# Kernel tuning notes

Measured on AMD Instinct MI355X. Metric: run time of the kernel, lower is better.

## Reference

```python
import jax, jax.numpy as jnp
import numpy as np

N = 6144
F_IN, H1, H2, EMB = 512, 256, 128, 64
ALPHA = 0.2  # LeakyReLU negative slope
NEG_INF = -9e15


def setup_inputs() -> dict:
    key = jax.random.key(0)
    ks = jax.random.split(key, 12)
    x = jax.random.normal(ks[0], (N, F_IN), dtype=jnp.float32)
    adj = (jax.random.uniform(ks[1], (N, N)) < 0.01).astype(jnp.float32)
    adj = jnp.maximum(adj, jnp.eye(N, dtype=jnp.float32))
    M = jax.random.uniform(ks[2], (N, N), dtype=jnp.float32)

    def glorot(k, shape):
        lim = float(np.sqrt(6.0 / (shape[0] + shape[1])))
        return jax.random.uniform(k, shape, jnp.float32, -lim, lim)

    params = {
        "W1": glorot(ks[3], (F_IN, H1)), "a_s1": glorot(ks[4], (H1, 1)), "a_n1": glorot(ks[5], (H1, 1)),
        "W2": glorot(ks[6], (H1, H2)),  "a_s2": glorot(ks[7], (H2, 1)), "a_n2": glorot(ks[8], (H2, 1)),
        "W3": glorot(ks[9], (H2, EMB)), "a_s3": glorot(ks[10], (EMB, 1)), "a_n3": glorot(ks[11], (EMB, 1)),
    }
    return {"x": x, "adj": adj, "M": M, **params}


def _gat_layer(x, adj, M, W, a_s, a_n):
    h = x @ W                                   # [N, d_out]
    e = (h @ a_s) + (h @ a_n).T                 # [N, N] pairwise logits
    e = jax.nn.leaky_relu(e * M, ALPHA)
    e = jnp.where(adj > 0, e, NEG_INF)
    att = jax.nn.softmax(e, axis=1)             # masked row softmax
    return jax.nn.elu(att @ h)


def reference(x, adj, M, W1, a_s1, a_n1, W2, a_s2, a_n2, W3, a_s3, a_n3):
    h = _gat_layer(x, adj, M, W1, a_s1, a_n1)
    h = _gat_layer(h, adj, M, W2, a_s2, a_n2)
    h = _gat_layer(h, adj, M, W3, a_s3, a_n3)
    z = h / jnp.maximum(jnp.linalg.norm(h, axis=1, keepdims=True), 1e-12)
    A_pred = jax.nn.sigmoid(z @ z.T)
    return (A_pred, z)
```

## Files before the change

### kernel.cpp

```cpp
#include <hip/hip_runtime.h>
#include <hip/hip_bf16.h>
#include <math.h>

#define NROW 6144
#define LRELU_ALPHA 0.2f
#define MAXD 128

typedef __attribute__((ext_vector_type(8))) __bf16 bf16x8;
typedef __attribute__((ext_vector_type(16))) float f32x16;

__global__ __launch_bounds__(256) void prep_scan(
    const float* __restrict__ adj, uint32_t* __restrict__ bm,
    const float* __restrict__ W1, const float* __restrict__ W2, const float* __restrict__ W3,
    __bf16* __restrict__ w1h, __bf16* __restrict__ w1l,
    __bf16* __restrict__ w2h, __bf16* __restrict__ w2l,
    __bf16* __restrict__ w3h, __bf16* __restrict__ w3l,
    const float* __restrict__ as1, const float* __restrict__ an1,
    const float* __restrict__ as2, const float* __restrict__ an2,
    const float* __restrict__ as3, const float* __restrict__ an3,
    float* __restrict__ wsa1, float* __restrict__ wna1,
    float* __restrict__ wsa2, float* __restrict__ wna2,
    float* __restrict__ wsa3, float* __restrict__ wna3) {
  int b = blockIdx.x;
  if (b < NROW) {
    const int id = b * 256 + threadIdx.x;
    const int row = id >> 8, sub = id & 255;
    const float4* ap = (const float4*)(adj + (size_t)row * NROW) + (sub >> 6) * 384 + (sub & 63);
    uint32_t mk = 0;
#pragma unroll
    for (int it = 0; it < 6; ++it) {
      float4 a = ap[it * 64];
      uint32_t q = (uint32_t)(a.x > 0.f) | ((uint32_t)(a.y > 0.f) << 1) |
                   ((uint32_t)(a.z > 0.f) << 2) | ((uint32_t)(a.w > 0.f) << 3);
      mk |= q << (it * 4);
    }
    bm[id] = mk;
    return;
  }
  b -= NROW;
  if (b < 672) {
    int idx = b * 256 + threadIdx.x;
    const float* W; __bf16 *wh, *wl; int K, D;
    if (idx < 131072) { W = W1; wh = w1h; wl = w1l; K = 512; D = 256; }
    else if (idx < 163840) { idx -= 131072; W = W2; wh = w2h; wl = w2l; K = 256; D = 128; }
    else { idx -= 163840; if (idx >= 8192) return; W = W3; wh = w3h; wl = w3l; K = 128; D = 64; }
    int k = idx / D, d = idx - k * D;
    float v = W[idx];
    __bf16 h = (__bf16)v;
    wh[(size_t)d * K + k] = h;
    wl[(size_t)d * K + k] = (__bf16)(v - (float)h);
    return;
  }
  int t = (b - 672) * 256 + threadIdx.x;
  if (t < 512) {
    float s = 0.f, n = 0.f;
    for (int d = 0; d < 256; ++d) { float w = W1[t * 256 + d]; s = fmaf(w, as1[d], s); n = fmaf(w, an1[d], n); }
    wsa1[t] = s; wna1[t] = n;
  } else if (t < 768) {
    int k = t - 512;
    float s = 0.f, n = 0.f;
    for (int d = 0; d < 128; ++d) { float w = W2[k * 128 + d]; s = fmaf(w, as2[d], s); n = fmaf(w, an2[d], n); }
    wsa2[k] = s; wna2[k] = n;
  } else if (t < 896) {
    int k = t - 768;
    float s = 0.f, n = 0.f;
    for (int d = 0; d < 64; ++d) { float w = W3[k * 64 + d]; s = fmaf(w, as3[d], s); n = fmaf(w, an3[d], n); }
    wsa3[k] = s; wna3[k] = n;
  }
}

__global__ __launch_bounds__(256) void csr_from_bitmap(const uint32_t* __restrict__ bm,
                                                       const float* __restrict__ Mm,
                                                       int* __restrict__ cnt,
                                                       int* __restrict__ cidx,
                                                       float* __restrict__ cmval) {
  const int row = blockIdx.x;
  const int tid = threadIdx.x, wv = tid >> 6, lane = tid & 63;
  __shared__ int wtot[4];
  __shared__ int jsh[MAXD];
  const uint32_t mask = bm[row * 256 + tid];
  const int pc = __popc(mask);
  int pre = pc;
#pragma unroll
  for (int off = 1; off < 64; off <<= 1) {
    int t = __shfl_up(pre, off);
    if (lane >= off) pre += t;
  }
  if (lane == 63) wtot[wv] = pre;
  __syncthreads();
  int base = pre - pc;
  for (int w = 0; w < wv; ++w) base += wtot[w];
  const int total = min(wtot[0] + wtot[1] + wtot[2] + wtot[3], MAXD);
  uint32_t m = mask;
  int p = base;
  const int cb0 = wv * 1536 + lane * 4;
  while (m) {
    int bit = __ffs(m) - 1;
    m &= m - 1;
    if (p < MAXD) jsh[p] = cb0 + ((bit >> 2) << 8) + (bit & 3);
    ++p;
  }
  __syncthreads();
  const float* mrow = Mm + (size_t)row * NROW;
  for (int k = tid; k < total; k += 256) {
    int j = jsh[k];
    cidx[(size_t)row * MAXD + k] = j;
    cmval[(size_t)row * MAXD + k] = mrow[j];
  }
  if (tid == 0) cnt[row] = total;
}

__global__ __launch_bounds__(256) void gemm_lds(
    const float* __restrict__ A,
    const __bf16* __restrict__ Bth, const __bf16* __restrict__ Btl,
    const float* __restrict__ wsa, const float* __restrict__ wna,
    float* __restrict__ sv, float* __restrict__ nv,
    float* __restrict__ C, __bf16* __restrict__ Cb, int K, int D) {
  __shared__ __bf16 Ah[64][72], Al[64][72], Bh[64][72], Bl[64][72];
  const int tid = threadIdx.x;
  const int wv = tid >> 6, lane = tid & 63;
  const int l31 = lane & 31, lh = lane >> 5;
  const int wr = wv >> 1, wc = wv & 1;
  const int rb = blockIdx.x * 64, jb = blockIdx.y * 64;
  const bool do_sn = (blockIdx.y == 0) && (wc == 0);
  f32x16 acc;
#pragma unroll
  for (int r = 0; r < 16; ++r) acc[r] = 0.f;
  float ss = 0.f, nn = 0.f;
  for (int kt = 0; kt < K; kt += 64) {
#pragma unroll
    for (int c2 = 0; c2 < 4; ++c2) {
      int flat = c2 * 256 + tid;
      int row = flat >> 4, cq = (flat & 15) * 4;
      float4 a = *(const float4*)(A + (size_t)(rb + row) * K + kt + cq);
      __bf16 h0 = (__bf16)a.x, h1 = (__bf16)a.y, h2 = (__bf16)a.z, h3 = (__bf16)a.w;
      Ah[row][cq] = h0; Ah[row][cq + 1] = h1; Ah[row][cq + 2] = h2; Ah[row][cq + 3] = h3;
      Al[row][cq] = (__bf16)(a.x - (float)h0);
      Al[row][cq + 1] = (__bf16)(a.y - (float)h1);
      Al[row][cq + 2] = (__bf16)(a.z - (float)h2);
      Al[row][cq + 3] = (__bf16)(a.w - (float)h3);
    }
#pragma unroll
    for (int c2 = 0; c2 < 2; ++c2) {
      int flat = c2 * 256 + tid;
      int row = flat >> 3, cq = (flat & 7) * 8;
      *(bf16x8*)&Bh[row][cq] = *(const bf16x8*)(Bth + (size_t)(jb + row) * K + kt + cq);
      *(bf16x8*)&Bl[row][cq] = *(const bf16x8*)(Btl + (size_t)(jb + row) * K + kt + cq);
    }
    __syncthreads();
#pragma unroll
    for (int kk = 0; kk < 4; ++kk) {
      bf16x8 af  = *(const bf16x8*)&Ah[wr * 32 + l31][kk * 16 + lh * 8];
      bf16x8 alf = *(const bf16x8*)&Al[wr * 32 + l31][kk * 16 + lh * 8];
      bf16x8 bhf = *(const bf16x8*)&Bh[wc * 32 + l31][kk * 16 + lh * 8];
      bf16x8 blf = *(const bf16x8*)&Bl[wc * 32 + l31][kk * 16 + lh * 8];
      if (do_sn) {
        const float* wsp = wsa + kt + kk * 16 + lh * 8;
        const float* wnp = wna + kt + kk * 16 + lh * 8;
#pragma unroll
        for (int t = 0; t < 8; ++t) {
          float av = (float)af[t] + (float)alf[t];
          ss = fmaf(av, wsp[t], ss);
          nn = fmaf(av, wnp[t], nn);
        }
      }
      acc = __builtin_amdgcn_mfma_f32_32x32x16_bf16(af, bhf, acc, 0, 0, 0);
      acc = __builtin_amdgcn_mfma_f32_32x32x16_bf16(af, blf, acc, 0, 0, 0);
      acc = __builtin_amdgcn_mfma_f32_32x32x16_bf16(alf, bhf, acc, 0, 0, 0);
    }
    __syncthreads();
  }
  if (do_sn) {
    ss += __shfl_xor(ss, 32);
    nn += __shfl_xor(nn, 32);
    if (lh == 0) { sv[rb + wr * 32 + l31] = ss; nv[rb + wr * 32 + l31] = nn; }
  }
#pragma unroll
  for (int r = 0; r < 16; ++r) {
    int rowi = (r & 3) + 8 * (r >> 2) + 4 * lh + wr * 32;
    int col = jb + wc * 32 + l31;
    if (C)  C[(size_t)(rb + rowi) * D + col] = acc[r];
    if (Cb) Cb[(size_t)(rb + rowi) * D + col] = (__bf16)acc[r];
  }
}

template <int D, int WPR, bool BF16G, bool NORM>
__global__ __launch_bounds__(256) void attn_csr(const float* __restrict__ h,
                                                const __bf16* __restrict__ hb,
                                                const int* __restrict__ cnt,
                                                const int* __restrict__ cidx,
                                                const float* __restrict__ cmval,
                                                const float* __restrict__ sv,
                                                const float* __restrict__ nv,
                                                float* __restrict__ out,
                                                __bf16* __restrict__ zb) {
  constexpr int RPB = 4 / WPR;
  constexpr int CW = D / WPR;
  constexpr int NQ = BF16G ? 2 : CW / 64;
  __shared__ float ws[4][MAXD];
  __shared__ int js[4][MAXD];
  const int wv = threadIdx.x >> 6, lane = threadIdx.x & 63;
  const int row = blockIdx.x * RPB + wv / WPR;
  const int half = wv % WPR;
  const int c = cnt[row];
  const float si = sv[row];
  const size_t cb = (size_t)row * MAXD;

  float e0 = -1e30f, e1 = -1e30f;
  int j0 = 0, j1 = 0;
  if (lane < c) {
    j0 = cidx[cb + lane];
    float v = (si + nv[j0]) * cmval[cb + lane];
    e0 = v > 0.f ? v : LRELU_ALPHA * v;
  }
  if (lane + 64 < c) {
    j1 = cidx[cb + lane + 64];
    float v = (si + nv[j1]) * cmval[cb + lane + 64];
    e1 = v > 0.f ? v : LRELU_ALPHA * v;
  }
  float mx = fmaxf(e0, e1);
#pragma unroll
  for (int off = 32; off; off >>= 1) mx = fmaxf(mx, __shfl_xor(mx, off));
  float w0 = lane < c ? __expf(e0 - mx) : 0.f;
  float w1 = lane + 64 < c ? __expf(e1 - mx) : 0.f;
  float s = w0 + w1;
#pragma unroll
  for (int off = 32; off; off >>= 1) s += __shfl_xor(s, off);
  const float inv = 1.f / s;
  ws[wv][lane] = w0 * inv;
  ws[wv][lane + 64] = w1 * inv;
  js[wv][lane] = j0;
  js[wv][lane + 64] = j1;
  const int cbase = half * CW;
  float acc[NQ];
#pragma unroll
  for (int q = 0; q < NQ; ++q) acc[q] = 0.f;
  if (BF16G) {
#pragma unroll 8
    for (int k = 0; k < c; ++k) {
      const float wk = ws[wv][k];
      const uint32_t* hr = (const uint32_t*)(hb + (size_t)js[wv][k] * D + cbase);
      uint32_t v = hr[lane];
      acc[0] = fmaf(wk, __uint_as_float(v << 16), acc[0]);
      acc[1] = fmaf(wk, __uint_as_float(v & 0xffff0000u), acc[1]);
    }
    float2 o;
    o.x = acc[0] > 0.f ? acc[0] : expm1f(acc[0]);
    o.y = acc[1] > 0.f ? acc[1] : expm1f(acc[1]);
    *(float2*)(out + (size_t)row * D + cbase + lane * 2) = o;
  } else {
#pragma unroll 8
    for (int k = 0; k < c; ++k) {
      const float wk = ws[wv][k];
      const float* hr = h + (size_t)js[wv][k] * D + cbase;
#pragma unroll
      for (int q = 0; q < NQ; ++q) acc[q] = fmaf(wk, hr[lane + q * 64], acc[q]);
    }
    if (!NORM) {
#pragma unroll
      for (int q = 0; q < NQ; ++q) {
        float a = acc[q];
        out[(size_t)row * D + cbase + lane + q * 64] = a > 0.f ? a : expm1f(a);
      }
    } else {
      float a = acc[0];
      a = a > 0.f ? a : expm1f(a);
      float sq = a * a;
#pragma unroll
      for (int off = 32; off; off >>= 1) sq += __shfl_xor(sq, off);
      float zv = a / fmaxf(sqrtf(sq), 1e-12f);
      out[(size_t)row * 64 + lane] = zv;
      zb[(size_t)row * 64 + lane] = (__bf16)zv;
    }
  }
}

__global__ __launch_bounds__(256) void decoder_mfma(const __bf16* __restrict__ zb,
                                                    float* __restrict__ out) {
  const int wv = threadIdx.x >> 6, lane = threadIdx.x & 63;
  const int ib = blockIdx.y * 64 + (wv >> 1) * 32;
  const int jb = blockIdx.x * 64 + (wv & 1) * 32;
  const int l31 = lane & 31, lh = lane >> 5;
  const __bf16* Arow = zb + (size_t)(ib + l31) * 64 + lh * 8;
  const __bf16* Brow = zb + (size_t)(jb + l31) * 64 + lh * 8;
  f32x16 acc;
#pragma unroll
  for (int r = 0; r < 16; ++r) acc[r] = 0.f;
#pragma unroll
  for (int kk = 0; kk < 4; ++kk) {
    bf16x8 af = *(const bf16x8*)(Arow + kk * 16);
    bf16x8 bfv = *(const bf16x8*)(Brow + kk * 16);
    acc = __builtin_amdgcn_mfma_f32_32x32x16_bf16(af, bfv, acc, 0, 0, 0);
  }
#pragma unroll
  for (int r = 0; r < 16; ++r) {
    int rowi = (r & 3) + 8 * (r >> 2) + 4 * lh;
    float v = 1.f / (1.f + __expf(-acc[r]));
    out[(size_t)(ib + rowi) * NROW + jb + l31] = v;
  }
}

extern "C" void kernel_launch(void* const* d_in, const int* in_sizes, int n_in,
                              void* d_out, int out_size, void* d_ws, size_t ws_size,
                              hipStream_t stream) {
  const float* x   = (const float*)d_in[0];
  const float* adj = (const float*)d_in[1];
  const float* Mm  = (const float*)d_in[2];
  const float* W1  = (const float*)d_in[3];
  const float* as1 = (const float*)d_in[4];
  const float* an1 = (const float*)d_in[5];
  const float* W2  = (const float*)d_in[6];
  const float* as2 = (const float*)d_in[7];
  const float* an2 = (const float*)d_in[8];
  const float* W3  = (const float*)d_in[9];
  const float* as3 = (const float*)d_in[10];
  const float* an3 = (const float*)d_in[11];

  float* out = (float*)d_out;
  float* z = out + (size_t)NROW * NROW;

  float* wsp = (float*)d_ws;
  float* hA   = wsp;
  float* hB   = hA + (size_t)NROW * 256;
  float* sv   = hB + (size_t)NROW * 256;
  float* nv   = sv + NROW;
  float* cmv  = nv + NROW;
  int*   cix  = (int*)(cmv + (size_t)NROW * MAXD);
  int*   cct  = cix + (size_t)NROW * MAXD;
  __bf16* zb  = (__bf16*)(cct + NROW);
  __bf16* w1h = zb + (size_t)NROW * 64;
  __bf16* w1l = w1h + 512 * 256;
  __bf16* w2h = w1l + 512 * 256;
  __bf16* w2l = w2h + 256 * 128;
  __bf16* w3h = w2l + 256 * 128;
  __bf16* w3l = w3h + 128 * 64;
  float* wsa1 = (float*)(w3l + 128 * 64);
  float* wna1 = wsa1 + 512;
  float* wsa2 = wna1 + 512;
  float* wna2 = wsa2 + 256;
  float* wsa3 = wna2 + 256;
  float* wna3 = wsa3 + 128;
  __bf16* hAb = (__bf16*)(wna3 + 128);
  uint32_t* bmp = (uint32_t*)(hAb + (size_t)NROW * 256);

  dim3 b256(256);

  prep_scan<<<dim3(NROW + 676), b256, 0, stream>>>(
      adj, bmp, W1, W2, W3, w1h, w1l, w2h, w2l, w3h, w3l,
      as1, an1, as2, an2, as3, an3, wsa1, wna1, wsa2, wna2, wsa3, wna3);

  csr_from_bitmap<<<dim3(NROW), b256, 0, stream>>>(bmp, Mm, cct, cix, cmv);

  gemm_lds<<<dim3(NROW / 64, 256 / 64), b256, 0, stream>>>(x, w1h, w1l, wsa1, wna1, sv, nv, nullptr, hAb, 512, 256);
  attn_csr<256, 2, true, false><<<dim3(NROW / 2), b256, 0, stream>>>(nullptr, hAb, cct, cix, cmv, sv, nv, hB, nullptr);

  gemm_lds<<<dim3(NROW / 64, 128 / 64), b256, 0, stream>>>(hB, w2h, w2l, wsa2, wna2, sv, nv, nullptr, hAb, 256, 128);
  attn_csr<128, 1, true, false><<<dim3(NROW / 4), b256, 0, stream>>>(nullptr, hAb, cct, cix, cmv, sv, nv, hB, nullptr);

  gemm_lds<<<dim3(NROW / 64, 64 / 64), b256, 0, stream>>>(hB, w3h, w3l, wsa3, wna3, sv, nv, hA, nullptr, 128, 64);
  attn_csr<64, 1, false, true><<<dim3(NROW / 4), b256, 0, stream>>>(hA, nullptr, cct, cix, cmv, sv, nv, z, zb);

  decoder_mfma<<<dim3(NROW / 64, NROW / 64), b256, 0, stream>>>(zb, out);
}
```

Measured before the change: 175.0 us.

## Shrink GEMM tiles to 32x32 and split K across waves

The projection GEMM moves from 64x64 output tiles, where each wave owned one 32x32 quadrant, to 32x32 tiles where the four waves each take a 16-wide K slice of every 64-wide K step. Partial accumulators and the s/n attention-score partials are reduced through shared memory by wave 0 before the store. This launches four times as many blocks for these small GEMMs to fill the GPU better. In exchange it loses A/B tile reuse, reloads A for every column block, and adds an LDS reduction plus an extra barrier.

```diff
diff --git a/kernel.cpp b/kernel.cpp
--- a/kernel.cpp
+++ b/kernel.cpp
@@ -110,26 +110,27 @@
   if (tid == 0) cnt[row] = total;
 }
 
-__global__ __launch_bounds__(256) void gemm_lds(
+__global__ __launch_bounds__(256) void gemm_lds2(
     const float* __restrict__ A,
     const __bf16* __restrict__ Bth, const __bf16* __restrict__ Btl,
     const float* __restrict__ wsa, const float* __restrict__ wna,
     float* __restrict__ sv, float* __restrict__ nv,
     float* __restrict__ C, __bf16* __restrict__ Cb, int K, int D) {
-  __shared__ __bf16 Ah[64][72], Al[64][72], Bh[64][72], Bl[64][72];
+  __shared__ __bf16 Ah[32][72], Al[32][72], Bh[32][72], Bl[32][72];
+  __shared__ float reds[3][16][64];
+  __shared__ float svs[4][32], nvs[4][32];
   const int tid = threadIdx.x;
   const int wv = tid >> 6, lane = tid & 63;
   const int l31 = lane & 31, lh = lane >> 5;
-  const int wr = wv >> 1, wc = wv & 1;
-  const int rb = blockIdx.x * 64, jb = blockIdx.y * 64;
-  const bool do_sn = (blockIdx.y == 0) && (wc == 0);
+  const int rb = blockIdx.x * 32, jb = blockIdx.y * 32;
+  const bool do_sn = (blockIdx.y == 0);
   f32x16 acc;
 #pragma unroll
   for (int r = 0; r < 16; ++r) acc[r] = 0.f;
   float ss = 0.f, nn = 0.f;
   for (int kt = 0; kt < K; kt += 64) {
 #pragma unroll
-    for (int c2 = 0; c2 < 4; ++c2) {
+    for (int c2 = 0; c2 < 2; ++c2) {
       int flat = c2 * 256 + tid;
       int row = flat >> 4, cq = (flat & 15) * 4;
       float4 a = *(const float4*)(A + (size_t)(rb + row) * K + kt + cq);
@@ -140,23 +141,20 @@
       Al[row][cq + 2] = (__bf16)(a.z - (float)h2);
       Al[row][cq + 3] = (__bf16)(a.w - (float)h3);
     }
-#pragma unroll
-    for (int c2 = 0; c2 < 2; ++c2) {
-      int flat = c2 * 256 + tid;
-      int row = flat >> 3, cq = (flat & 7) * 8;
+    {
+      int row = tid >> 3, cq = (tid & 7) * 8;
       *(bf16x8*)&Bh[row][cq] = *(const bf16x8*)(Bth + (size_t)(jb + row) * K + kt + cq);
       *(bf16x8*)&Bl[row][cq] = *(const bf16x8*)(Btl + (size_t)(jb + row) * K + kt + cq);
     }
     __syncthreads();
-#pragma unroll
-    for (int kk = 0; kk < 4; ++kk) {
-      bf16x8 af  = *(const bf16x8*)&Ah[wr * 32 + l31][kk * 16 + lh * 8];
-      bf16x8 alf = *(const bf16x8*)&Al[wr * 32 + l31][kk * 16 + lh * 8];
-      bf16x8 bhf = *(const bf16x8*)&Bh[wc * 32 + l31][kk * 16 + lh * 8];
-      bf16x8 blf = *(const bf16x8*)&Bl[wc * 32 + l31][kk * 16 + lh * 8];
+    {
+      bf16x8 af  = *(const bf16x8*)&Ah[l31][wv * 16 + lh * 8];
+      bf16x8 alf = *(const bf16x8*)&Al[l31][wv * 16 + lh * 8];
+      bf16x8 bhf = *(const bf16x8*)&Bh[l31][wv * 16 + lh * 8];
+      bf16x8 blf = *(const bf16x8*)&Bl[l31][wv * 16 + lh * 8];
       if (do_sn) {
-        const float* wsp = wsa + kt + kk * 16 + lh * 8;
-        const float* wnp = wna + kt + kk * 16 + lh * 8;
+        const float* wsp = wsa + kt + wv * 16 + lh * 8;
+        const float* wnp = wna + kt + wv * 16 + lh * 8;
 #pragma unroll
         for (int t = 0; t < 8; ++t) {
           float av = (float)af[t] + (float)alf[t];
@@ -170,17 +168,35 @@
     }
     __syncthreads();
   }
+  if (wv > 0) {
+#pragma unroll
+    for (int r = 0; r < 16; ++r) reds[wv - 1][r][lane] = acc[r];
+  }
   if (do_sn) {
     ss += __shfl_xor(ss, 32);
     nn += __shfl_xor(nn, 32);
-    if (lh == 0) { sv[rb + wr * 32 + l31] = ss; nv[rb + wr * 32 + l31] = nn; }
-  }
-#pragma unroll
-  for (int r = 0; r < 16; ++r) {
-    int rowi = (r & 3) + 8 * (r >> 2) + 4 * lh + wr * 32;
-    int col = jb + wc * 32 + l31;
-    if (C)  C[(size_t)(rb + rowi) * D + col] = acc[r];
-    if (Cb) Cb[(size_t)(rb + rowi) * D + col] = (__bf16)acc[r];
+    if (lh == 0) { svs[wv][l31] = ss; nvs[wv][l31] = nn; }
+  }
+  __syncthreads();
+  if (wv == 0) {
+#pragma unroll
+    for (int w = 0; w < 3; ++w)
+#pragma unroll
+      for (int r = 0; r < 16; ++r) acc[r] += reds[w][r][lane];
+    if (do_sn && lh == 0) {
+      float s = 0.f, n = 0.f;
+#pragma unroll
+      for (int w = 0; w < 4; ++w) { s += svs[w][l31]; n += nvs[w][l31]; }
+      sv[rb + l31] = s;
+      nv[rb + l31] = n;
+    }
+#pragma unroll
+    for (int r = 0; r < 16; ++r) {
+      int rowi = (r & 3) + 8 * (r >> 2) + 4 * lh;
+      int col = jb + l31;
+      if (C)  C[(size_t)(rb + rowi) * D + col] = acc[r];
+      if (Cb) Cb[(size_t)(rb + rowi) * D + col] = (__bf16)acc[r];
+    }
   }
 }
 
@@ -351,13 +367,13 @@
 
   csr_from_bitmap<<<dim3(NROW), b256, 0, stream>>>(bmp, Mm, cct, cix, cmv);
 
-  gemm_lds<<<dim3(NROW / 64, 256 / 64), b256, 0, stream>>>(x, w1h, w1l, wsa1, wna1, sv, nv, nullptr, hAb, 512, 256);
+  gemm_lds2<<<dim3(NROW / 32, 256 / 32), b256, 0, stream>>>(x, w1h, w1l, wsa1, wna1, sv, nv, nullptr, hAb, 512, 256);
   attn_csr<256, 2, true, false><<<dim3(NROW / 2), b256, 0, stream>>>(nullptr, hAb, cct, cix, cmv, sv, nv, hB, nullptr);
 
-  gemm_lds<<<dim3(NROW / 64, 128 / 64), b256, 0, stream>>>(hB, w2h, w2l, wsa2, wna2, sv, nv, nullptr, hAb, 256, 128);
+  gemm_lds2<<<dim3(NROW / 32, 128 / 32), b256, 0, stream>>>(hB, w2h, w2l, wsa2, wna2, sv, nv, nullptr, hAb, 256, 128);
   attn_csr<128, 1, true, false><<<dim3(NROW / 4), b256, 0, stream>>>(nullptr, hAb, cct, cix, cmv, sv, nv, hB, nullptr);
 
-  gemm_lds<<<dim3(NROW / 64, 64 / 64), b256, 0, stream>>>(hB, w3h, w3l, wsa3, wna3, sv, nv, hA, nullptr, 128, 64);
+  gemm_lds2<<<dim3(NROW / 32, 64 / 32), b256, 0, stream>>>(hB, w3h, w3l, wsa3, wna3, sv, nv, hA, nullptr, 128, 64);
   attn_csr<64, 1, false, true><<<dim3(NROW / 4), b256, 0, stream>>>(hA, nullptr, cct, cix, cmv, sv, nv, z, zb);
 
   decoder_mfma<<<dim3(NROW / 64, NROW / 64), b256, 0, stream>>>(zb, out);
```

New measurement: 171.4 us, median of 2. 1.02x faster.
